# Performance work log

Hardware: AMD Instinct MI355X
Metric: run time of the kernel (lower is better)

The kernel has to match this reference:

```python
import jax, jax.numpy as jnp
import numpy as np

B, N, D = 2, 2048, 1024
H = 16
HD = D // H  # 64
N_CTX = 256


def setup_inputs() -> dict:
    key = jax.random.key(0)
    ks = jax.random.split(key, 10)
    x = jax.random.normal(ks[0], (B, N, D), dtype=jnp.float32)
    ctx_ppr = jax.random.uniform(ks[1], (N_CTX,), dtype=jnp.float32, minval=1e-4, maxval=1.0)
    ctx_trust = jax.random.uniform(ks[2], (N_CTX,), dtype=jnp.float32)
    attn_mask = jax.random.randint(ks[3], (N, N), 0, 2).astype(jnp.bool_)
    # parameters (nn.Linear convention: y = x @ W.T + b)
    s_in = 1.0 / np.sqrt(D)
    W_in = jax.random.uniform(ks[4], (3 * D, D), dtype=jnp.float32, minval=-s_in, maxval=s_in)
    b_in = jax.random.uniform(ks[5], (3 * D,), dtype=jnp.float32, minval=-s_in, maxval=s_in)
    W_out = jax.random.uniform(ks[6], (D, D), dtype=jnp.float32, minval=-s_in, maxval=s_in)
    b_out = jax.random.uniform(ks[7], (D,), dtype=jnp.float32, minval=-s_in, maxval=s_in)
    log_ppr_alpha = jnp.ones((1,), jnp.float32) * 0.1
    trust_scale = jnp.ones((1,), jnp.float32) * 0.1
    return {"x": x, "ctx_ppr": ctx_ppr, "ctx_trust": ctx_trust, "n_ctx": N_CTX,
            "attn_mask": attn_mask, "W_in": W_in, "b_in": b_in,
            "W_out": W_out, "b_out": b_out,
            "log_ppr_alpha": log_ppr_alpha, "trust_scale": trust_scale}


def reference(x, ctx_ppr, ctx_trust, n_ctx, attn_mask, W_in, b_in, W_out, b_out,
              log_ppr_alpha, trust_scale):
    Bx, Nx, Dx = x.shape
    scale = HD ** -0.5
    qkv = x @ W_in.T + b_in  # [B,N,3D]
    q, k, v = jnp.split(qkv, 3, axis=-1)
    q = q.reshape(Bx, Nx, H, HD).transpose(0, 2, 1, 3)  # [B,H,N,d]
    k = k.reshape(Bx, Nx, H, HD).transpose(0, 2, 1, 3)
    v = v.reshape(Bx, Nx, H, HD).transpose(0, 2, 1, 3)
    if n_ctx > 0:
        gate = jax.nn.sigmoid(trust_scale[0] * ctx_trust)  # [n_ctx]
        gate_full = jnp.concatenate([gate, jnp.ones(Nx - n_ctx, x.dtype)])
        v = v * gate_full[None, None, :, None]
    logits = jnp.einsum('bhqd,bhkd->bhqk', q, k) * scale
    if n_ctx > 0:
        bias = log_ppr_alpha[0] * jnp.log(jnp.clip(ctx_ppr, 1e-8, None))
        col_bias = jnp.concatenate([bias, jnp.zeros(Nx - n_ctx, x.dtype)])
        logits = logits + col_bias[None, None, None, :]
    logits = jnp.where(attn_mask[None, None, :, :], -jnp.inf, logits)
    weights = jax.nn.softmax(logits, axis=-1)
    out = jnp.einsum('bhqk,bhkd->bhqd', weights, v)
    out = out.transpose(0, 2, 1, 3).reshape(Bx, Nx, Dx)
    return out @ W_out.T + b_out
```

## Files before the change

### kernel.cpp

```cpp
#include <hip/hip_runtime.h>
#include <hip/hip_bf16.h>
#include <hip/hip_fp16.h>
#include <math.h>

#define B_   2
#define N_   2048
#define D_   1024
#define H_   16
#define TD_  3072
#define LOG2E 1.44269504088896340736f
#define SCALE_Q (0.125f * LOG2E)

typedef short  bf16x8 __attribute__((ext_vector_type(8)));
typedef _Float16 f16x8 __attribute__((ext_vector_type(8)));
typedef float  f32x4  __attribute__((ext_vector_type(4)));
typedef float  f32x16 __attribute__((ext_vector_type(16)));

#define MFMA16(a, b, c)   __builtin_amdgcn_mfma_f32_16x16x32_bf16(a, b, c, 0, 0, 0)
#define MFMA32B(a, b, c)  __builtin_amdgcn_mfma_f32_32x32x16_bf16(a, b, c, 0, 0, 0)
#define MFMA32H(a, b, c)  __builtin_amdgcn_mfma_f32_32x32x16_f16(a, b, c, 0, 0, 0)

__device__ __forceinline__ ushort f2bf(float f) {
    union { float f; unsigned u; } v; v.f = f;
    unsigned r = (v.u + 0x7fffu + ((v.u >> 16) & 1u)) >> 16;
    return (ushort)r;
}
__device__ __forceinline__ unsigned pkrtz(float a, float b) {
    typedef __fp16 h2 __attribute__((ext_vector_type(2)));
    union { h2 h; unsigned u; } c;
    c.h = __builtin_amdgcn_cvt_pkrtz(a, b);
    return c.u;
}
__device__ __forceinline__ void async16(const void* g, void* l) {
    __builtin_amdgcn_global_load_lds(
        (const __attribute__((address_space(1))) unsigned*)g,
        (__attribute__((address_space(3))) unsigned*)l, 16, 0, 0);
}

__global__ __launch_bounds__(256) void preprocess(
    const float* __restrict__ x, const float* __restrict__ W_in,
    const float* __restrict__ W_out, const float* __restrict__ ctx_ppr,
    const float* __restrict__ log_alpha, const int* __restrict__ n_ctx_p,
    const int* __restrict__ mask,
    ushort* __restrict__ xb, ushort* __restrict__ wib, ushort* __restrict__ wob,
    float* __restrict__ term)
{
    const int J0 = 1048576, J1 = 786432, J2 = 262144, JT = 1048576;
    int t = blockIdx.x * 256 + threadIdx.x;
    if (t < J0 + J1 + J2) {
        const float* src; ushort* dst; int i = t;
        if (i < J0)           { src = x;      dst = xb;  }
        else if (i < J0 + J1) { i -= J0;      src = W_in;  dst = wib; }
        else                  { i -= J0 + J1; src = W_out; dst = wob; }
        float4 v = ((const float4*)src)[i];
        ushort4 o;
        o.x = f2bf(v.x); o.y = f2bf(v.y); o.z = f2bf(v.z); o.w = f2bf(v.w);
        ((ushort4*)dst)[i] = o;
    } else if (t < J0 + J1 + J2 + JT) {
        int i = t - (J0 + J1 + J2);
        int k4 = (i & 511) * 4;
        int4 m = ((const int4*)mask)[i];
        int nc = n_ctx_p[0];
        float al = log_alpha[0];
        float4 o;
        float bv[4];
        #pragma unroll
        for (int j = 0; j < 4; ++j) {
            int k = k4 + j;
            bv[j] = (k < nc) ? (al * __log2f(fmaxf(ctx_ppr[k], 1e-8f)) - 4.f) : -4.f;
        }
        o.x = m.x ? -1e30f : bv[0];
        o.y = m.y ? -1e30f : bv[1];
        o.z = m.z ? -1e30f : bv[2];
        o.w = m.w ? -1e30f : bv[3];
        ((float4*)term)[i] = o;
    }
}

template<int BCOL, int MODE>
__global__ __launch_bounds__(256) void gemm_bt(
    const ushort* __restrict__ A, const ushort* __restrict__ Bw,
    const float* __restrict__ bias, float* __restrict__ Cf,
    ushort* __restrict__ Ch, int Ncol, int K,
    const float* __restrict__ ctx_trust, const float* __restrict__ trust_scale,
    const int* __restrict__ n_ctx_p)
{
    constexpr int NT = BCOL / 32;
    __shared__ ushort tA[128 * 32];
    __shared__ ushort tB[BCOL * 32];
    const int tid = threadIdx.x;
    const int lane = tid & 63, wv = tid >> 6;
    const int ln = lane & 15, kg = lane >> 4;
    const int rh = wv >> 1, ch = wv & 1;
    const int row0 = blockIdx.y * 128, col0 = blockIdx.x * BCOL;

    int offA[4], offB[NT];
    #pragma unroll
    for (int i = 0; i < 4; ++i) {
        int ra = rh * 64 + i * 16 + ln;
        offA[i] = ra * 32 + ((kg ^ ((ra >> 1) & 3)) << 3);
    }
    #pragma unroll
    for (int i = 0; i < NT; ++i) {
        int rb = ch * (BCOL / 2) + i * 16 + ln;
        offB[i] = rb * 32 + ((kg ^ ((rb >> 1) & 3)) << 3);
    }
    f32x4 acc[4][NT];
    #pragma unroll
    for (int i = 0; i < 4; ++i)
        #pragma unroll
        for (int j = 0; j < NT; ++j) acc[i][j] = (f32x4){0.f, 0.f, 0.f, 0.f};

    for (int kt = 0; kt < K; kt += 32) {
        __syncthreads();
        #pragma unroll
        for (int r2 = 0; r2 < 2; ++r2) {
            int g = r2 * 256 + tid;
            int row = g >> 2;
            int srck = ((g & 3) ^ ((row >> 1) & 3)) << 3;
            async16(A + (size_t)(row0 + row) * K + kt + srck, &tA[g * 8]);
        }
        #pragma unroll
        for (int r2 = 0; r2 < BCOL / 64; ++r2) {
            int g = r2 * 256 + tid;
            int row = g >> 2;
            int srck = ((g & 3) ^ ((row >> 1) & 3)) << 3;
            async16(Bw + (size_t)(col0 + row) * K + kt + srck, &tB[g * 8]);
        }
        __syncthreads();
        bf16x8 af[4], bfr[NT];
        #pragma unroll
        for (int i = 0; i < 4; ++i)  af[i]  = *(const bf16x8*)&tA[offA[i]];
        #pragma unroll
        for (int i = 0; i < NT; ++i) bfr[i] = *(const bf16x8*)&tB[offB[i]];
        #pragma unroll
        for (int mt = 0; mt < 4; ++mt)
            #pragma unroll
            for (int nt = 0; nt < NT; ++nt)
                acc[mt][nt] = MFMA16(af[mt], bfr[nt], acc[mt][nt]);
    }

    const int nctx = n_ctx_p ? n_ctx_p[0] : 0;
    const float ts = trust_scale ? trust_scale[0] : 0.f;
    #pragma unroll
    for (int nt = 0; nt < NT; ++nt) {
        int col = col0 + ch * (BCOL / 2) + nt * 16 + ln;
        float cbv = (MODE != 2) ? bias[col] : 0.f;
        float gmul = 1.f;
        if (MODE == 2) {
            int tok = col & (N_ - 1);
            if (tok < nctx)
                gmul = 1.f / (1.f + __expf(-ts * ctx_trust[tok]));
        }
        #pragma unroll
        for (int mt = 0; mt < 4; ++mt) {
            int rbase = row0 + rh * 64 + mt * 16 + kg * 4;
            f32x4 a = acc[mt][nt];
            if (MODE == 0) {
                #pragma unroll
                for (int reg = 0; reg < 4; ++reg)
                    Cf[(size_t)(rbase + reg) * Ncol + col] = a[reg] + cbv;
            } else if (MODE == 1) {
                const float qs = (col < D_) ? SCALE_Q : 1.f;
                #pragma unroll
                for (int reg = 0; reg < 4; ++reg)
                    Ch[(size_t)(rbase + reg) * Ncol + col] = f2bf((a[reg] + cbv) * qs);
            } else {
                f32x4 bv4 = *(const f32x4*)&bias[rbase];
                #pragma unroll
                for (int reg = 0; reg < 4; ++reg) {
                    float v = (a[reg] + bv4[reg]) * gmul;
                    _Float16 hv = (_Float16)v;
                    union { _Float16 h; ushort u; } cv; cv.h = hv;
                    Ch[((size_t)((col >> 11) * 1024 + rbase + reg)) * 2048 + (col & (N_ - 1))] = cv.u;
                }
            }
        }
    }
}

__global__ __launch_bounds__(512, 4) void attn(
    const ushort* __restrict__ qkb,
    const _Float16* __restrict__ vT,
    const float* __restrict__ term,
    ushort* __restrict__ attb)
{
    __shared__ ushort   Kt[2][64 * 64];
    __shared__ _Float16 Vt[2][64 * 64];
    const int tid = threadIdx.x;
    const int lane = tid & 63, wv = tid >> 6;
    const int q31 = lane & 31, hi = lane >> 5;
    const int bh = blockIdx.x;
    const int b = bh >> 4, h = bh & 15;
    const int q = blockIdx.y * 256 + wv * 32 + q31;

    bf16x8 qf[4];
    {
        const ushort* qrow = qkb + (size_t)(b * N_ + q) * 2048 + h * 64;
        #pragma unroll
        for (int ks = 0; ks < 4; ++ks)
            qf[ks] = *(const bf16x8*)(qrow + ks * 16 + hi * 8);
    }
    const size_t kgbase = (size_t)(b * N_) * 2048 + 1024 + h * 64;
    const _Float16* vbase = vT + (size_t)(b * 1024 + h * 64) * 2048;
    const float* trow = term + (size_t)q * 2048;

    f32x16 O[2];
    O[0] = (f32x16)(0.f); O[1] = (f32x16)(0.f);
    float lrun = 0.f;

    {
        int g = tid; int row = g >> 3;
        int sg = (g & 7) ^ ((row ^ (row >> 3)) & 7);
        async16(qkb + kgbase + (size_t)row * 2048 + sg * 8, &Kt[0][g * 8]);
        async16(vbase + (size_t)row * 2048 + sg * 8, &Vt[0][g * 8]);
    }

    int fsw[2];
    #pragma unroll
    for (int t = 0; t < 2; ++t) {
        int row = t * 32 + q31;
        fsw[t] = (row ^ (row >> 3)) & 7;
    }

    for (int ci = 0; ci < 32; ++ci) {
        const int c0 = ci * 64;
        __syncthreads();
        if (ci < 31) {
            const int c1 = c0 + 64, nb = (ci + 1) & 1;
            int g = tid; int row = g >> 3;
            int sg = (g & 7) ^ ((row ^ (row >> 3)) & 7);
            async16(qkb + kgbase + (size_t)(c1 + row) * 2048 + sg * 8, &Kt[nb][g * 8]);
            async16(vbase + (size_t)row * 2048 + c1 + sg * 8, &Vt[nb][g * 8]);
        }
        const ushort*   KT = Kt[ci & 1];
        const _Float16* VT = Vt[ci & 1];

        f32x4 tm[2][4];
        #pragma unroll
        for (int t = 0; t < 2; ++t)
            #pragma unroll
            for (int g = 0; g < 4; ++g)
                tm[t][g] = *(const f32x4*)(trow + c0 + t * 32 + g * 8 + hi * 4);

        f32x16 S[2];
        S[0] = (f32x16)(0.f); S[1] = (f32x16)(0.f);
        #pragma unroll
        for (int t = 0; t < 2; ++t) {
            const int rbase = (t * 32 + q31) * 64;
            #pragma unroll
            for (int ks = 0; ks < 4; ++ks) {
                bf16x8 kf = *(const bf16x8*)&KT[rbase + (((ks * 2 + hi) ^ fsw[t]) << 3)];
                S[t] = MFMA32B(kf, qf[ks], S[t]);
            }
        }

        unsigned pk[2][8];
        __half2 hs0 = __float2half2_rn(0.f), hs1 = __float2half2_rn(0.f);
        #pragma unroll
        for (int t = 0; t < 2; ++t) {
            float p[16];
            #pragma unroll
            for (int g = 0; g < 4; ++g)
                #pragma unroll
                for (int r = 0; r < 4; ++r) {
                    const int reg = g * 4 + r;
                    p[reg] = __builtin_exp2f(S[t][reg] + tm[t][g][r]);
                }
            #pragma unroll
            for (int i = 0; i < 8; ++i) {
                pk[t][i] = pkrtz(p[2 * i], p[2 * i + 1]);
                union { unsigned u; __half2 h; } c; c.u = pk[t][i];
                if (i & 1) hs1 = __hadd2(hs1, c.h); else hs0 = __hadd2(hs0, c.h);
            }
        }
        {
            __half2 hs = __hadd2(hs0, hs1);
            lrun += __low2float(hs) + __high2float(hs);
        }

        #pragma unroll
        for (int ks = 0; ks < 4; ++ks) {
            const int t = ks >> 1, lo4 = (ks & 1) * 4;
            unsigned u0 = pk[t][lo4 + 0], u1 = pk[t][lo4 + 1];
            unsigned u2 = pk[t][lo4 + 2], u3 = pk[t][lo4 + 3];
            unsigned own0 = hi ? u2 : u0, own1 = hi ? u3 : u1;
            unsigned snd0 = hi ? u0 : u2, snd1 = hi ? u1 : u3;
            unsigned rv0 = (unsigned)__shfl_xor((int)snd0, 32);
            unsigned rv1 = (unsigned)__shfl_xor((int)snd1, 32);
            union { f16x8 v; unsigned u[4]; } frag;
            frag.u[0] = hi ? rv0 : own0;
            frag.u[1] = hi ? rv1 : own1;
            frag.u[2] = hi ? own0 : rv0;
            frag.u[3] = hi ? own1 : rv1;
            #pragma unroll
            for (int t2 = 0; t2 < 2; ++t2) {
                const int vb = (t2 * 32 + q31) * 64;
                union { f16x8 v; int4 i; } vf;
                vf.i = *(const int4*)&VT[vb + (((ks * 2 + hi) ^ fsw[t2]) << 3)];
                O[t2] = MFMA32H(vf.v, frag.v, O[t2]);
            }
        }
    }

    float l = lrun + __shfl_xor(lrun, 32);
    float inv = 1.f / l;
    ushort* orow = attb + (size_t)(b * N_ + q) * 1024 + h * 64;
    #pragma unroll
    for (int t = 0; t < 2; ++t)
        #pragma unroll
        for (int g = 0; g < 4; ++g) {
            ushort4 o;
            #pragma unroll
            for (int r = 0; r < 4; ++r)
                ((ushort*)&o)[r] = f2bf(O[t][g * 4 + r] * inv);
            *(ushort4*)&orow[t * 32 + g * 8 + hi * 4] = o;
        }
}

extern "C" void kernel_launch(void* const* d_in, const int* in_sizes, int n_in,
                              void* d_out, int out_size, void* d_ws, size_t ws_size,
                              hipStream_t stream)
{
    const float* x         = (const float*)d_in[0];
    const float* ctx_ppr   = (const float*)d_in[1];
    const float* ctx_trust = (const float*)d_in[2];
    const int*   n_ctx_p   = (const int*)d_in[3];
    const int*   attn_mask = (const int*)d_in[4];
    const float* W_in      = (const float*)d_in[5];
    const float* b_in      = (const float*)d_in[6];
    const float* W_out     = (const float*)d_in[7];
    const float* b_out     = (const float*)d_in[8];
    const float* log_alpha = (const float*)d_in[9];
    const float* trust_sc  = (const float*)d_in[10];
    float* out = (float*)d_out;

    char* ws = (char*)d_ws;
    ushort*    xb     = (ushort*)ws;    ws += (size_t)4096 * 1024 * 2;
    ushort*    wib    = (ushort*)ws;    ws += (size_t)3072 * 1024 * 2;
    ushort*    wob    = (ushort*)ws;    ws += (size_t)1024 * 1024 * 2;
    ushort*    qkb    = (ushort*)ws;    ws += (size_t)4096 * 2048 * 2;
    _Float16*  vT     = (_Float16*)ws;  ws += (size_t)2048 * 2048 * 2;
    ushort*    attbuf = (ushort*)ws;    ws += (size_t)4096 * 1024 * 2;
    float*     term   = (float*)ws;     ws += (size_t)2048 * 2048 * 4;

    hipLaunchKernelGGL(preprocess, dim3(12288), dim3(256), 0, stream,
                       x, W_in, W_out, ctx_ppr, log_alpha, n_ctx_p, attn_mask,
                       xb, wib, wob, term);

    hipLaunchKernelGGL((gemm_bt<128, 1>), dim3(16, 32), dim3(256), 0, stream,
                       xb, wib, b_in, (float*)nullptr, qkb, 2048, 1024,
                       (const float*)nullptr, (const float*)nullptr, (const int*)nullptr);

    hipLaunchKernelGGL((gemm_bt<64, 2>), dim3(64, 8), dim3(256), 0, stream,
                       wib + (size_t)2048 * 1024, xb, b_in + 2 * D_, (float*)nullptr,
                       (ushort*)vT, 4096, 1024, ctx_trust, trust_sc, n_ctx_p);

    hipLaunchKernelGGL(attn, dim3(32, 8), dim3(512), 0, stream,
                       qkb, vT, term, attbuf);

    hipLaunchKernelGGL((gemm_bt<64, 0>), dim3(16, 32), dim3(256), 0, stream,
                       attbuf, wob, b_out, out, (ushort*)nullptr, 1024, 1024,
                       (const float*)nullptr, (const float*)nullptr, (const int*)nullptr);
}
```

Measured before the change: 290.5 us.

## Split attention over two key halves and combine partials in a separate kernel

The attention kernel now runs with a third grid dimension of 2, and each block processes only half of the 2048 keys. Unnormalized fp32 partial outputs and row sums go to a workspace. A new combine kernel adds the two halves, normalizes, and writes the bf16 attention buffer. The aim is to double the block count so the 256-block grid fills more CUs, at the cost of extra fp32 partial-result traffic and an added kernel launch.

```diff
diff --git a/kernel.cpp b/kernel.cpp
--- a/kernel.cpp
+++ b/kernel.cpp
@@ -183,7 +183,8 @@
     const ushort* __restrict__ qkb,
     const _Float16* __restrict__ vT,
     const float* __restrict__ term,
-    ushort* __restrict__ attb)
+    float* __restrict__ pO,
+    float* __restrict__ pl)
 {
     __shared__ ushort   Kt[2][64 * 64];
     __shared__ _Float16 Vt[2][64 * 64];
@@ -192,6 +193,8 @@
     const int q31 = lane & 31, hi = lane >> 5;
     const int bh = blockIdx.x;
     const int b = bh >> 4, h = bh & 15;
+    const int z = blockIdx.z;
+    const int k0z = z * 1024;
     const int q = blockIdx.y * 256 + wv * 32 + q31;
 
     bf16x8 qf[4];
@@ -203,7 +206,7 @@
     }
     const size_t kgbase = (size_t)(b * N_) * 2048 + 1024 + h * 64;
     const _Float16* vbase = vT + (size_t)(b * 1024 + h * 64) * 2048;
-    const float* trow = term + (size_t)q * 2048;
+    const float* trow = term + (size_t)q * 2048 + k0z;
 
     f32x16 O[2];
     O[0] = (f32x16)(0.f); O[1] = (f32x16)(0.f);
@@ -212,8 +215,8 @@
     {
         int g = tid; int row = g >> 3;
         int sg = (g & 7) ^ ((row ^ (row >> 3)) & 7);
-        async16(qkb + kgbase + (size_t)row * 2048 + sg * 8, &Kt[0][g * 8]);
-        async16(vbase + (size_t)row * 2048 + sg * 8, &Vt[0][g * 8]);
+        async16(qkb + kgbase + (size_t)(k0z + row) * 2048 + sg * 8, &Kt[0][g * 8]);
+        async16(vbase + (size_t)row * 2048 + k0z + sg * 8, &Vt[0][g * 8]);
     }
 
     int fsw[2];
@@ -223,15 +226,15 @@
         fsw[t] = (row ^ (row >> 3)) & 7;
     }
 
-    for (int ci = 0; ci < 32; ++ci) {
+    for (int ci = 0; ci < 16; ++ci) {
         const int c0 = ci * 64;
         __syncthreads();
-        if (ci < 31) {
+        if (ci < 15) {
             const int c1 = c0 + 64, nb = (ci + 1) & 1;
             int g = tid; int row = g >> 3;
             int sg = (g & 7) ^ ((row ^ (row >> 3)) & 7);
-            async16(qkb + kgbase + (size_t)(c1 + row) * 2048 + sg * 8, &Kt[nb][g * 8]);
-            async16(vbase + (size_t)row * 2048 + c1 + sg * 8, &Vt[nb][g * 8]);
+            async16(qkb + kgbase + (size_t)(k0z + c1 + row) * 2048 + sg * 8, &Kt[nb][g * 8]);
+            async16(vbase + (size_t)row * 2048 + k0z + c1 + sg * 8, &Vt[nb][g * 8]);
         }
         const ushort*   KT = Kt[ci & 1];
         const _Float16* VT = Vt[ci & 1];
@@ -303,19 +306,37 @@
         }
     }
 
+    float* obase = pO + (((size_t)(z * 32 + bh) * 2048) + q) * 64;
+    #pragma unroll
+    for (int t = 0; t < 2; ++t)
+        #pragma unroll
+        for (int g = 0; g < 4; ++g) {
+            f32x4 o4 = { O[t][g * 4 + 0], O[t][g * 4 + 1], O[t][g * 4 + 2], O[t][g * 4 + 3] };
+            *(f32x4*)(obase + t * 32 + g * 8 + hi * 4) = o4;
+        }
     float l = lrun + __shfl_xor(lrun, 32);
+    if (hi == 0)
+        pl[(size_t)(z * 32 + bh) * 2048 + q] = l;
+}
+
+__global__ __launch_bounds__(256) void combine(
+    const float* __restrict__ pO, const float* __restrict__ pl,
+    ushort* __restrict__ attb)
+{
+    int i = blockIdx.x * 256 + threadIdx.x;
+    int bhq = i >> 4, d4 = (i & 15) << 2;
+    const float* o0 = pO + (size_t)bhq * 64 + d4;
+    const float* o1 = o0 + (size_t)32 * 2048 * 64;
+    float l = pl[bhq] + pl[bhq + 32 * 2048];
     float inv = 1.f / l;
-    ushort* orow = attb + (size_t)(b * N_ + q) * 1024 + h * 64;
-    #pragma unroll
-    for (int t = 0; t < 2; ++t)
-        #pragma unroll
-        for (int g = 0; g < 4; ++g) {
-            ushort4 o;
-            #pragma unroll
-            for (int r = 0; r < 4; ++r)
-                ((ushort*)&o)[r] = f2bf(O[t][g * 4 + r] * inv);
-            *(ushort4*)&orow[t * 32 + g * 8 + hi * 4] = o;
-        }
+    f32x4 a = *(const f32x4*)o0;
+    f32x4 b = *(const f32x4*)o1;
+    ushort4 o;
+    #pragma unroll
+    for (int r = 0; r < 4; ++r)
+        ((ushort*)&o)[r] = f2bf((a[r] + b[r]) * inv);
+    int bh = bhq >> 11, q = bhq & 2047;
+    *(ushort4*)&attb[((size_t)((bh >> 4) * 2048 + q)) * 1024 + (bh & 15) * 64 + d4] = o;
 }
 
 extern "C" void kernel_launch(void* const* d_in, const int* in_sizes, int n_in,
@@ -343,6 +364,8 @@
     _Float16*  vT     = (_Float16*)ws;  ws += (size_t)2048 * 2048 * 2;
     ushort*    attbuf = (ushort*)ws;    ws += (size_t)4096 * 1024 * 2;
     float*     term   = (float*)ws;     ws += (size_t)2048 * 2048 * 4;
+    float*     pO     = (float*)ws;     ws += (size_t)2 * 32 * 2048 * 64 * 4;
+    float*     pl     = (float*)ws;     ws += (size_t)2 * 32 * 2048 * 4;
 
     hipLaunchKernelGGL(preprocess, dim3(12288), dim3(256), 0, stream,
                        x, W_in, W_out, ctx_ppr, log_alpha, n_ctx_p, attn_mask,
@@ -356,8 +379,11 @@
                        wib + (size_t)2048 * 1024, xb, b_in + 2 * D_, (float*)nullptr,
                        (ushort*)vT, 4096, 1024, ctx_trust, trust_sc, n_ctx_p);
 
-    hipLaunchKernelGGL(attn, dim3(32, 8), dim3(512), 0, stream,
-                       qkb, vT, term, attbuf);
+    hipLaunchKernelGGL(attn, dim3(32, 8, 2), dim3(512), 0, stream,
+                       qkb, vT, term, pO, pl);
+
+    hipLaunchKernelGGL(combine, dim3(4096), dim3(256), 0, stream,
+                       pO, pl, attbuf);
 
     hipLaunchKernelGGL((gemm_bt<64, 0>), dim3(16, 32), dim3(256), 0, stream,
                        attbuf, wob, b_out, out, (ushort*)nullptr, 1024, 1024,
```

New measurement: 269.1 us. -7.4%, faster.
